# Performance work log

Measured on AMD Instinct MI355X. Metric: run time of the kernel, lower is better.

Reference implementation:

```python
import jax, jax.numpy as jnp
import numpy as np

N = 50000      # nodes
E = 800000     # edges (avg degree 16)
EMB = 128      # emb_dim
NF = 7         # x_features
EF = 5         # edge_features
L = 5          # num_layer
BN_EPS = 1e-5


def setup_inputs() -> dict:
    key = jax.random.key(0)
    ks = jax.random.split(key, 12)
    s = 0.05
    return {
        "x": jax.random.normal(ks[0], (N, NF), jnp.float32),
        "edge_attr": jax.random.normal(ks[1], (E, EF), jnp.float32),
        "edge_index": jax.random.randint(ks[2], (2, E), 0, N, dtype=jnp.int32),
        "W_x": jax.random.normal(ks[3], (NF, EMB), jnp.float32) * s,
        "b_x": jax.random.normal(ks[4], (NF, EMB), jnp.float32) * s,
        "W_e": jax.random.normal(ks[5], (L, EF, EMB), jnp.float32) * s,
        "b_e": jax.random.normal(ks[6], (L, EF, EMB), jnp.float32) * s,
        # per-layer GIN update MLP: Linear(EMB,2EMB)-ReLU-Linear(2EMB,EMB)
        "W1": jax.random.normal(ks[7], (L, EMB, 2 * EMB), jnp.float32) * s,
        "b1": jnp.zeros((L, 2 * EMB), jnp.float32),
        "W2": jax.random.normal(ks[8], (L, 2 * EMB, EMB), jnp.float32) * s,
        "b2": jnp.zeros((L, EMB), jnp.float32),
        # per-layer BatchNorm1d affine params
        "gamma": jnp.ones((L, EMB), jnp.float32),
        "beta": jnp.zeros((L, EMB), jnp.float32),
    }


def reference(x, edge_attr, W_x, b_x, W_e, b_e, W1, b1, W2, b2, gamma, beta, edge_index):
    src, dst = edge_index[0], edge_index[1]
    # initial node embedding: sum of 7 Linear(1,EMB) applied per column == x @ W_x + sum(biases)
    h = x @ W_x + b_x.sum(axis=0)  # [N, EMB]
    for l in range(L):
        # edge embeddings: sum of EF Linear(1,EMB) over edge_attr columns
        e_emb = edge_attr @ W_e[l] + b_e[l].sum(axis=0)  # [E, EMB]
        sl_emb = b_e[l].sum(axis=0)  # self-loop edges have zero attr -> bias sum
        # message = x_j + edge_emb, aggr = add (scatter over dst); self loops add h + sl_emb
        msg = h[src] + e_emb                                        # [E, EMB]
        agg = jax.ops.segment_sum(msg, dst, num_segments=N) + h + sl_emb  # [N, EMB]
        # GIN update MLP
        z = jax.nn.relu(agg @ W1[l] + b1[l]) @ W2[l] + b2[l]        # [N, EMB]
        # BatchNorm1d (training-mode batch stats, biased variance)
        mu = z.mean(axis=0)
        var = z.var(axis=0)
        z = (z - mu) * jax.lax.rsqrt(var + BN_EPS) * gamma[l] + beta[l]
        # ELU on all but last layer; dropout is identity at drop_ratio=0; JK='last'
        h = jax.nn.elu(z) if l < L - 1 else z
    return h
```

## Files before the change

kernel.cpp:

```cpp
#include <hip/hip_runtime.h>
#include <math.h>

#define NN 50000
#define NE 800000
#define EMB 128
#define HID 256
#define NF 7
#define EF 5
#define NL 5
#define BN_EPS 1e-5f
#define NREP 32
#define SCAN_B 196

typedef __attribute__((ext_vector_type(8))) short bf16x8;
typedef __attribute__((ext_vector_type(4))) float f32x4;

__device__ inline unsigned short f2b(float f) {
    unsigned u = __builtin_bit_cast(unsigned, f);
    return (unsigned short)((u + 0x7fffu + ((u >> 16) & 1u)) >> 16);
}
__device__ inline float b2f(unsigned us) {
    return __builtin_bit_cast(float, us << 16);
}
__device__ inline void split2(float a, float b, unsigned& hi, unsigned& lo) {
    unsigned short ha = f2b(a), hb = f2b(b);
    unsigned short la = f2b(a - b2f(ha)), lb = f2b(b - b2f(hb));
    hi = (unsigned)ha | ((unsigned)hb << 16);
    lo = (unsigned)la | ((unsigned)lb << 16);
}
__device__ inline unsigned pkh2(float a, float b) {
    union { unsigned v; _Float16 h[2]; } x;
    x.h[0] = (_Float16)a; x.h[1] = (_Float16)b;
    return x.v;
}
__device__ inline float2 uph2(unsigned u) {
    union { unsigned v; _Float16 h[2]; } x; x.v = u;
    return make_float2((float)x.h[0], (float)x.h[1]);
}

__global__ void k_prep(const float* __restrict__ b_x, const float* __restrict__ b_e,
                       float* __restrict__ bsum_x, float* __restrict__ bsum_e,
                       int* __restrict__ counts, int* __restrict__ cursor) {
    int tid = threadIdx.x;
    if (blockIdx.x == 0 && tid < EMB) {
        float s = 0.f;
        for (int f = 0; f < NF; ++f) s += b_x[f * EMB + tid];
        bsum_x[tid] = s;
        for (int l = 0; l < NL; ++l) {
            float se = 0.f;
            for (int f = 0; f < EF; ++f) se += b_e[(l * EF + f) * EMB + tid];
            bsum_e[l * EMB + tid] = se;
        }
    }
    int gid = blockIdx.x * blockDim.x + tid;
    int stride = gridDim.x * blockDim.x;
    for (int i = gid; i < NN; i += stride) { counts[i] = 0; cursor[i] = 0; }
}

__global__ void k_prepw(const float* __restrict__ W1, const float* __restrict__ W2,
                        unsigned short* __restrict__ W1ph, unsigned short* __restrict__ W1pl,
                        unsigned short* __restrict__ W2ph, unsigned short* __restrict__ W2pl) {
    const int TOT = NL * EMB * HID;
    int gid = blockIdx.x * blockDim.x + threadIdx.x;
    if (gid < TOT) {
        int l = gid / (EMB * HID);
        int r = gid % (EMB * HID);
        int w = r >> 13;
        int rem = r & 8191;
        int h2 = rem >> 11;
        int rem2 = rem & 2047;
        int kk = rem2 >> 9;
        int rem3 = rem2 & 511;
        int lane = rem3 >> 3;
        int j = rem3 & 7;
        int hc = w * 64 + h2 * 16 + (lane & 15);
        int k = kk * 32 + (lane >> 4) * 8 + j;
        float wv = W1[((size_t)l * EMB + k) * HID + hc];
        unsigned short hi = f2b(wv);
        W1ph[gid] = hi;
        W1pl[gid] = f2b(wv - b2f(hi));
    } else if (gid < 2 * TOT) {
        int g = gid - TOT;
        int l = g / (EMB * HID);
        int r = g % (EMB * HID);
        int w = r >> 13;
        int rem = r & 8191;
        int o2 = rem >> 12;
        int rem2 = rem & 4095;
        int kk = rem2 >> 9;
        int rem3 = rem2 & 511;
        int lane = rem3 >> 3;
        int j = rem3 & 7;
        int oc = w * 32 + o2 * 16 + (lane & 15);
        int k2 = kk * 32 + (lane >> 4) * 8 + j;
        float wv = W2[((size_t)l * HID + k2) * EMB + oc];
        unsigned short hi = f2b(wv);
        W2ph[g] = hi;
        W2pl[g] = f2b(wv - b2f(hi));
    }
}

__global__ void k_init(const float* __restrict__ x, const float* __restrict__ W_x,
                       const float* __restrict__ bsum_x, unsigned short* __restrict__ h16) {
    int gid = blockIdx.x * blockDim.x + threadIdx.x;
    int v = gid >> 5;
    if (v >= NN) return;
    int c = (gid & 31) << 2;
    float4 acc = *(const float4*)(bsum_x + c);
    #pragma unroll
    for (int f = 0; f < NF; ++f) {
        float xv = x[(size_t)v * NF + f];
        float4 w = *(const float4*)(W_x + f * EMB + c);
        acc.x += xv * w.x; acc.y += xv * w.y; acc.z += xv * w.z; acc.w += xv * w.w;
    }
    uint2 p = make_uint2(pkh2(acc.x, acc.y), pkh2(acc.z, acc.w));
    *(uint2*)(h16 + (size_t)v * EMB + c) = p;
}

__global__ void k_hist(const int* __restrict__ dst, int* __restrict__ counts) {
    int e = blockIdx.x * blockDim.x + threadIdx.x;
    if (e < NE) atomicAdd(&counts[dst[e]], 1);
}

__global__ void k_scan1(const int* __restrict__ counts, int* __restrict__ bsum) {
    int tid = threadIdx.x;
    int i = blockIdx.x * 256 + tid;
    int v = (i < NN) ? counts[i] : 0;
    #pragma unroll
    for (int off = 1; off < 64; off <<= 1) v += __shfl_xor(v, off, 64);
    __shared__ int ws[4];
    if ((tid & 63) == 0) ws[tid >> 6] = v;
    __syncthreads();
    if (tid == 0) bsum[blockIdx.x] = ws[0] + ws[1] + ws[2] + ws[3];
}

__global__ void k_scan2(const int* __restrict__ bsum, int* __restrict__ bpre,
                        int* __restrict__ row_start) {
    int tid = threadIdx.x;
    int x = (tid < SCAN_B) ? bsum[tid] : 0;
    int lane = tid & 63, wv = tid >> 6;
    int v = x;
    #pragma unroll
    for (int off = 1; off < 64; off <<= 1) {
        int t = __shfl_up(v, off, 64);
        if (lane >= off) v += t;
    }
    __shared__ int wsum[4];
    if (lane == 63) wsum[wv] = v;
    __syncthreads();
    int woff = 0;
    #pragma unroll
    for (int w = 0; w < 4; ++w) if (w < wv) woff += wsum[w];
    int incl = v + woff;
    if (tid < SCAN_B) bpre[tid] = incl - x;
    if (tid == 255) row_start[NN] = incl;
}

__global__ void k_scan3(const int* __restrict__ counts, const int* __restrict__ bpre,
                        int* __restrict__ row_start) {
    int tid = threadIdx.x;
    int i = blockIdx.x * 256 + tid;
    int x = (i < NN) ? counts[i] : 0;
    int lane = tid & 63, wv = tid >> 6;
    int v = x;
    #pragma unroll
    for (int off = 1; off < 64; off <<= 1) {
        int t = __shfl_up(v, off, 64);
        if (lane >= off) v += t;
    }
    __shared__ int wsum[4];
    if (lane == 63) wsum[wv] = v;
    __syncthreads();
    int woff = 0;
    #pragma unroll
    for (int w = 0; w < 4; ++w) if (w < wv) woff += wsum[w];
    if (i < NN) row_start[i] = bpre[blockIdx.x] + v + woff - x;
}

__global__ void k_fill(const int* __restrict__ src, const int* __restrict__ dst,
                       const float* __restrict__ edge_attr,
                       const int* __restrict__ row_start, int* __restrict__ cursor,
                       uint4* __restrict__ sorted_pk) {
    int e = blockIdx.x * blockDim.x + threadIdx.x;
    if (e >= NE) return;
    int d = dst[e];
    int pos = atomicAdd(&cursor[d], 1);
    int idx = row_start[d] + pos;
    const float* ea = edge_attr + (size_t)e * EF;
    float a0 = ea[0], a1 = ea[1], a2 = ea[2], a3 = ea[3], a4 = ea[4];
    uint4 pk;
    pk.x = (unsigned)src[e];
    pk.y = pkh2(a0, a1);
    pk.z = pkh2(a2, a3);
    pk.w = pkh2(a4, 0.f);
    sorted_pk[idx] = pk;
}

__global__ void k_esum(const uint4* __restrict__ sorted_pk,
                       const int* __restrict__ row_start,
                       float* __restrict__ attsum, int* __restrict__ sorted_srcc) {
    int v = blockIdx.x * blockDim.x + threadIdx.x;
    if (v >= NN) return;
    int e0 = row_start[v], e1 = row_start[v + 1];
    float s0 = 0.f, s1 = 0.f, s2 = 0.f, s3 = 0.f, s4 = 0.f;
    for (int e = e0; e < e1; ++e) {
        uint4 pk = sorted_pk[e];
        sorted_srcc[e] = (int)pk.x;
        float2 a01 = uph2(pk.y), a23 = uph2(pk.z), a4x = uph2(pk.w);
        s0 += a01.x; s1 += a01.y; s2 += a23.x; s3 += a23.y; s4 += a4x.x;
    }
    float* o = attsum + (size_t)v * 8;
    *(float4*)(o) = make_float4(s0, s1, s2, s3);
    *(float4*)(o + 4) = make_float4(s4, (float)(e1 - e0), 0.f, 0.f);
}

template<int APPLY_BN>
__global__ __launch_bounds__(256) void k_agg(
        const unsigned short* __restrict__ st16, const int* __restrict__ sorted_srcc,
        const float* __restrict__ attsum, const float* __restrict__ scsh,
        const float* __restrict__ W_e_l, const float* __restrict__ bsum_e_l,
        const int* __restrict__ row_start,
        unsigned* __restrict__ agg_hi, unsigned* __restrict__ agg_lo,
        float* __restrict__ stats) {
    int tid = threadIdx.x;
    if (blockIdx.x < NREP) stats[blockIdx.x * 2 * EMB + tid] = 0.f;
    int gid = blockIdx.x * 256 + tid;
    int v = gid >> 6;
    if (v >= NN) return;
    int c = (gid & 63) << 1;
    float2 we0 = *(const float2*)(W_e_l + 0 * EMB + c);
    float2 we1 = *(const float2*)(W_e_l + 1 * EMB + c);
    float2 we2 = *(const float2*)(W_e_l + 2 * EMB + c);
    float2 we3 = *(const float2*)(W_e_l + 3 * EMB + c);
    float2 we4 = *(const float2*)(W_e_l + 4 * EMB + c);
    float2 bs = *(const float2*)(bsum_e_l + c);
    float2 sc2 = make_float2(0.f, 0.f), sh2 = make_float2(0.f, 0.f);
    if (APPLY_BN) {
        sc2 = *(const float2*)(scsh + c);
        sh2 = *(const float2*)(scsh + EMB + c);
    }
    auto state = [&](unsigned u) -> float2 {
        float2 t = uph2(u);
        if (APPLY_BN) {
            t.x = t.x * sc2.x + sh2.x;
            t.y = t.y * sc2.y + sh2.y;
            t.x = (t.x > 0.f) ? t.x : (__expf(t.x) - 1.f);
            t.y = (t.y > 0.f) ? t.y : (__expf(t.y) - 1.f);
        }
        return t;
    };
    float2 hv = state(*(const unsigned*)(st16 + (size_t)v * EMB + c));
    const float* at = attsum + (size_t)v * 8;
    float4 a03 = *(const float4*)(at);
    float2 a45 = *(const float2*)(at + 4);
    float ax = hv.x + (a45.y + 1.f) * bs.x
             + a03.x*we0.x + a03.y*we1.x + a03.z*we2.x + a03.w*we3.x + a45.x*we4.x;
    float ay = hv.y + (a45.y + 1.f) * bs.y
             + a03.x*we0.y + a03.y*we1.y + a03.z*we2.y + a03.w*we3.y + a45.x*we4.y;
    int e0 = row_start[v], e1 = row_start[v + 1];
    int e = e0;
    for (; e + 8 <= e1; e += 8) {
        int s0 = __builtin_amdgcn_readfirstlane(sorted_srcc[e + 0]);
        int s1 = __builtin_amdgcn_readfirstlane(sorted_srcc[e + 1]);
        int s2 = __builtin_amdgcn_readfirstlane(sorted_srcc[e + 2]);
        int s3 = __builtin_amdgcn_readfirstlane(sorted_srcc[e + 3]);
        int s4 = __builtin_amdgcn_readfirstlane(sorted_srcc[e + 4]);
        int s5 = __builtin_amdgcn_readfirstlane(sorted_srcc[e + 5]);
        int s6 = __builtin_amdgcn_readfirstlane(sorted_srcc[e + 6]);
        int s7 = __builtin_amdgcn_readfirstlane(sorted_srcc[e + 7]);
        unsigned u0 = *(const unsigned*)(st16 + (size_t)s0 * EMB + c);
        unsigned u1 = *(const unsigned*)(st16 + (size_t)s1 * EMB + c);
        unsigned u2 = *(const unsigned*)(st16 + (size_t)s2 * EMB + c);
        unsigned u3 = *(const unsigned*)(st16 + (size_t)s3 * EMB + c);
        unsigned u4 = *(const unsigned*)(st16 + (size_t)s4 * EMB + c);
        unsigned u5 = *(const unsigned*)(st16 + (size_t)s5 * EMB + c);
        unsigned u6 = *(const unsigned*)(st16 + (size_t)s6 * EMB + c);
        unsigned u7 = *(const unsigned*)(st16 + (size_t)s7 * EMB + c);
        float2 h0 = state(u0), h1 = state(u1), h2 = state(u2), h3 = state(u3);
        float2 h4 = state(u4), h5 = state(u5), h6 = state(u6), h7 = state(u7);
        ax += ((h0.x + h1.x) + (h2.x + h3.x)) + ((h4.x + h5.x) + (h6.x + h7.x));
        ay += ((h0.y + h1.y) + (h2.y + h3.y)) + ((h4.y + h5.y) + (h6.y + h7.y));
    }
    for (; e < e1; ++e) {
        int s = __builtin_amdgcn_readfirstlane(sorted_srcc[e]);
        float2 hs = state(*(const unsigned*)(st16 + (size_t)s * EMB + c));
        ax += hs.x;
        ay += hs.y;
    }
    unsigned phi, plo;
    split2(ax, ay, phi, plo);
    size_t o = (size_t)v * (EMB / 2) + (c >> 1);
    agg_hi[o] = phi;
    agg_lo[o] = plo;
}

__global__ __launch_bounds__(256) void k_mlp(
        const unsigned short* __restrict__ aggh, const unsigned short* __restrict__ aggl,
        const unsigned short* __restrict__ W1ph, const unsigned short* __restrict__ W1pl,
        const float* __restrict__ b1_l,
        const unsigned short* __restrict__ W2ph, const unsigned short* __restrict__ W2pl,
        const float* __restrict__ b2_l,
        unsigned short* __restrict__ z16, float* __restrict__ stats) {
    __shared__ unsigned short Ahi[32][136];
    __shared__ unsigned short Alo[32][136];
    __shared__ unsigned short Hhi[32][264];
    __shared__ unsigned short Hlo[32][264];
    int tid = threadIdx.x;
    int r0 = blockIdx.x * 32;
    int rep = blockIdx.x & (NREP - 1);
    #pragma unroll
    for (int it = 0; it < 4; ++it) {
        int idx = it * 256 + tid;
        int plane = idx >> 9;
        int k = idx & 511;
        int row = k >> 4;
        int cb = (k & 15) * 8;
        int grow = r0 + row;
        uint4 val = make_uint4(0u, 0u, 0u, 0u);
        const unsigned short* srcp = plane ? aggl : aggh;
        if (grow < NN) val = *(const uint4*)(srcp + (size_t)grow * EMB + cb);
        if (plane) *(uint4*)(&Alo[row][cb]) = val;
        else       *(uint4*)(&Ahi[row][cb]) = val;
    }
    __syncthreads();
    int wave = tid >> 6, lane = tid & 63;
    int l16 = lane & 15, quad = lane >> 4;
    {
        bf16x8 ahi[2][4], alo[2][4];
        #pragma unroll
        for (int nt = 0; nt < 2; ++nt)
            #pragma unroll
            for (int kk = 0; kk < 4; ++kk) {
                ahi[nt][kk] = *(const bf16x8*)(&Ahi[nt * 16 + l16][kk * 32 + quad * 8]);
                alo[nt][kk] = *(const bf16x8*)(&Alo[nt * 16 + l16][kk * 32 + quad * 8]);
            }
        #pragma unroll
        for (int h2 = 0; h2 < 4; ++h2) {
            bf16x8 whi[4], wlo[4];
            #pragma unroll
            for (int kk = 0; kk < 4; ++kk) {
                size_t off = ((((size_t)(wave * 4 + h2) * 4) + kk) * 64 + lane) * 8;
                whi[kk] = *(const bf16x8*)(W1ph + off);
                wlo[kk] = *(const bf16x8*)(W1pl + off);
            }
            float4 bv = *(const float4*)(b1_l + wave * 64 + h2 * 16 + quad * 4);
            f32x4 bias = {bv.x, bv.y, bv.z, bv.w};
            #pragma unroll
            for (int nt = 0; nt < 2; ++nt) {
                f32x4 acc = bias;
                #pragma unroll
                for (int kk = 0; kk < 4; ++kk)
                    acc = __builtin_amdgcn_mfma_f32_16x16x32_bf16(whi[kk], ahi[nt][kk], acc, 0, 0, 0);
                #pragma unroll
                for (int kk = 0; kk < 4; ++kk)
                    acc = __builtin_amdgcn_mfma_f32_16x16x32_bf16(whi[kk], alo[nt][kk], acc, 0, 0, 0);
                #pragma unroll
                for (int kk = 0; kk < 4; ++kk)
                    acc = __builtin_amdgcn_mfma_f32_16x16x32_bf16(wlo[kk], ahi[nt][kk], acc, 0, 0, 0);
                float v0 = fmaxf(acc[0], 0.f), v1 = fmaxf(acc[1], 0.f);
                float v2 = fmaxf(acc[2], 0.f), v3 = fmaxf(acc[3], 0.f);
                unsigned hiA, loA, hiB, loB;
                split2(v0, v1, hiA, loA);
                split2(v2, v3, hiB, loB);
                int col = wave * 64 + h2 * 16 + quad * 4;
                *(uint2*)(&Hhi[nt * 16 + l16][col]) = make_uint2(hiA, hiB);
                *(uint2*)(&Hlo[nt * 16 + l16][col]) = make_uint2(loA, loB);
            }
        }
    }
    __syncthreads();
    float ss[2][4] = {}, sq[2][4] = {};
    #pragma unroll
    for (int o2 = 0; o2 < 2; ++o2) {
        bf16x8 w2h[8], w2l[8];
        #pragma unroll
        for (int kk = 0; kk < 8; ++kk) {
            size_t off = ((((size_t)(wave * 2 + o2) * 8) + kk) * 64 + lane) * 8;
            w2h[kk] = *(const bf16x8*)(W2ph + off);
            w2l[kk] = *(const bf16x8*)(W2pl + off);
        }
        float4 bv = *(const float4*)(b2_l + wave * 32 + o2 * 16 + quad * 4);
        f32x4 bias = {bv.x, bv.y, bv.z, bv.w};
        #pragma unroll
        for (int nt = 0; nt < 2; ++nt) {
            bf16x8 hh[8], hl[8];
            #pragma unroll
            for (int kk = 0; kk < 8; ++kk) {
                hh[kk] = *(const bf16x8*)(&Hhi[nt * 16 + l16][kk * 32 + quad * 8]);
                hl[kk] = *(const bf16x8*)(&Hlo[nt * 16 + l16][kk * 32 + quad * 8]);
            }
            f32x4 acc = bias;
            #pragma unroll
            for (int kk = 0; kk < 8; ++kk)
                acc = __builtin_amdgcn_mfma_f32_16x16x32_bf16(w2h[kk], hh[kk], acc, 0, 0, 0);
            #pragma unroll
            for (int kk = 0; kk < 8; ++kk)
                acc = __builtin_amdgcn_mfma_f32_16x16x32_bf16(w2h[kk], hl[kk], acc, 0, 0, 0);
            #pragma unroll
            for (int kk = 0; kk < 8; ++kk)
                acc = __builtin_amdgcn_mfma_f32_16x16x32_bf16(w2l[kk], hh[kk], acc, 0, 0, 0);
            int node = r0 + nt * 16 + l16;
            if (node < NN) {
                uint2 p = make_uint2(pkh2(acc[0], acc[1]), pkh2(acc[2], acc[3]));
                *(uint2*)(z16 + (size_t)node * EMB + wave * 32 + o2 * 16 + quad * 4) = p;
                #pragma unroll
                for (int r = 0; r < 4; ++r) {
                    ss[o2][r] += acc[r];
                    sq[o2][r] += acc[r] * acc[r];
                }
            }
        }
    }
    #pragma unroll
    for (int o2 = 0; o2 < 2; ++o2)
        #pragma unroll
        for (int r = 0; r < 4; ++r) {
            float s = ss[o2][r], q = sq[o2][r];
            #pragma unroll
            for (int m = 1; m < 16; m <<= 1) {
                s += __shfl_xor(s, m, 64);
                q += __shfl_xor(q, m, 64);
            }
            if (l16 == 0) {
                int oc = wave * 32 + o2 * 16 + quad * 4 + r;
                atomicAdd(&stats[rep * 2 * EMB + oc], s);
                atomicAdd(&stats[rep * 2 * EMB + EMB + oc], q);
            }
        }
}

__global__ void k_bnscale(const float* __restrict__ stats,
                          const float* __restrict__ gamma_l, const float* __restrict__ beta_l,
                          float* __restrict__ scsh) {
    int tid = threadIdx.x;
    float s = 0.f, q = 0.f;
    #pragma unroll
    for (int r = 0; r < NREP; ++r) {
        s += stats[r * 2 * EMB + tid];
        q += stats[r * 2 * EMB + EMB + tid];
    }
    float mu = s * (1.f / NN);
    float var = q * (1.f / NN) - mu * mu;
    float sf = gamma_l[tid] * rsqrtf(var + BN_EPS);
    scsh[tid] = sf;
    scsh[EMB + tid] = beta_l[tid] - mu * sf;
}

__global__ void k_bn(const unsigned short* __restrict__ z16, const float* __restrict__ scsh,
                     float* __restrict__ fout) {
    __shared__ float sc[EMB], sh[EMB];
    int tid = threadIdx.x;
    if (tid < EMB) {
        sc[tid] = scsh[tid];
        sh[tid] = scsh[EMB + tid];
    }
    __syncthreads();
    int gid = blockIdx.x * blockDim.x + tid;
    if (gid >= NN * EMB / 4) return;
    int c = (gid & 31) << 2;
    uint2 zp = *(const uint2*)(z16 + (size_t)gid * 4);
    float2 z01 = uph2(zp.x), z23 = uph2(zp.y);
    float o0 = z01.x * sc[c + 0] + sh[c + 0];
    float o1 = z01.y * sc[c + 1] + sh[c + 1];
    float o2 = z23.x * sc[c + 2] + sh[c + 2];
    float o3 = z23.y * sc[c + 3] + sh[c + 3];
    *(float4*)(fout + (size_t)gid * 4) = make_float4(o0, o1, o2, o3);
}

extern "C" void kernel_launch(void* const* d_in, const int* in_sizes, int n_in,
                              void* d_out, int out_size, void* d_ws, size_t ws_size,
                              hipStream_t stream) {
    const float* x         = (const float*)d_in[0];
    const float* edge_attr = (const float*)d_in[1];
    const int*   edge_idx  = (const int*)d_in[2];
    const float* W_x   = (const float*)d_in[3];
    const float* b_x   = (const float*)d_in[4];
    const float* W_e   = (const float*)d_in[5];
    const float* b_e   = (const float*)d_in[6];
    const float* W1    = (const float*)d_in[7];
    const float* b1    = (const float*)d_in[8];
    const float* W2    = (const float*)d_in[9];
    const float* b2    = (const float*)d_in[10];
    const float* gamma = (const float*)d_in[11];
    const float* beta  = (const float*)d_in[12];
    float* fout = (float*)d_out;

    const int* src = edge_idx;
    const int* dst = edge_idx + NE;

    char* p = (char*)d_ws;
    auto alloc = [&](size_t bytes) { char* q = p; p += (bytes + 255) & ~(size_t)255; return q; };
    unsigned short* h16 = (unsigned short*)alloc((size_t)NN * EMB * 2);
    unsigned short* z16 = (unsigned short*)alloc((size_t)NN * EMB * 2);
    unsigned* agg_hi = (unsigned*)alloc((size_t)NN * EMB * 2);
    unsigned* agg_lo = (unsigned*)alloc((size_t)NN * EMB * 2);
    unsigned short* W1ph = (unsigned short*)alloc((size_t)NL * HID * EMB * 2);
    unsigned short* W1pl = (unsigned short*)alloc((size_t)NL * HID * EMB * 2);
    unsigned short* W2ph = (unsigned short*)alloc((size_t)NL * EMB * HID * 2);
    unsigned short* W2pl = (unsigned short*)alloc((size_t)NL * EMB * HID * 2);
    int*   row_start  = (int*)alloc((NN + 1) * sizeof(int));
    int*   counts     = (int*)alloc(NN * sizeof(int));
    int*   cursor     = (int*)alloc(NN * sizeof(int));
    uint4* sorted_pk  = (uint4*)alloc((size_t)NE * sizeof(uint4));
    int*   sorted_srcc= (int*)alloc((size_t)NE * sizeof(int));
    float* attsum     = (float*)alloc((size_t)NN * 8 * sizeof(float));
    int*   bsum       = (int*)alloc(SCAN_B * sizeof(int));
    int*   bpre       = (int*)alloc(SCAN_B * sizeof(int));
    float* stats      = (float*)alloc((size_t)NREP * 2 * EMB * sizeof(float));
    float* scsh       = (float*)alloc(2 * EMB * sizeof(float));
    float* bsum_x     = (float*)alloc(EMB * sizeof(float));
    float* bsum_e     = (float*)alloc(NL * EMB * sizeof(float));

    k_prep<<<256, 256, 0, stream>>>(b_x, b_e, bsum_x, bsum_e, counts, cursor);
    k_prepw<<<(2 * NL * EMB * HID + 255) / 256, 256, 0, stream>>>(W1, W2, W1ph, W1pl, W2ph, W2pl);
    k_init<<<(NN * 32 + 255) / 256, 256, 0, stream>>>(x, W_x, bsum_x, h16);
    k_hist<<<(NE + 255) / 256, 256, 0, stream>>>(dst, counts);
    k_scan1<<<SCAN_B, 256, 0, stream>>>(counts, bsum);
    k_scan2<<<1, 256, 0, stream>>>(bsum, bpre, row_start);
    k_scan3<<<SCAN_B, 256, 0, stream>>>(counts, bpre, row_start);
    k_fill<<<(NE + 255) / 256, 256, 0, stream>>>(src, dst, edge_attr, row_start, cursor,
                                                 sorted_pk);
    k_esum<<<SCAN_B, 256, 0, stream>>>(sorted_pk, row_start, attsum, sorted_srcc);
    const int AGG_GRID = (NN * 64 + 255) / 256;
    for (int l = 0; l < NL; ++l) {
        if (l == 0) {
            k_agg<0><<<AGG_GRID, 256, 0, stream>>>(
                h16, sorted_srcc, attsum, scsh,
                W_e + (size_t)l * EF * EMB, bsum_e + l * EMB, row_start,
                agg_hi, agg_lo, stats);
        } else {
            k_agg<1><<<AGG_GRID, 256, 0, stream>>>(
                z16, sorted_srcc, attsum, scsh,
                W_e + (size_t)l * EF * EMB, bsum_e + l * EMB, row_start,
                agg_hi, agg_lo, stats);
        }
        k_mlp<<<(NN + 31) / 32, 256, 0, stream>>>(
            (const unsigned short*)agg_hi, (const unsigned short*)agg_lo,
            W1ph + (size_t)l * HID * EMB, W1pl + (size_t)l * HID * EMB, b1 + (size_t)l * HID,
            W2ph + (size_t)l * EMB * HID, W2pl + (size_t)l * EMB * HID, b2 + (size_t)l * EMB,
            z16, stats);
        k_bnscale<<<1, 128, 0, stream>>>(stats, gamma + l * EMB, beta + l * EMB, scsh);
    }
    k_bn<<<(NN * EMB / 4 + 255) / 256, 256, 0, stream>>>(z16, scsh, fout);
}
```

Measured before the change: 634.6 us.

## Gather 16-byte neighbor rows across four lane-groups and fold edge-attr sums into fill

The aggregation kernel now splits each 64-lane wavefront into four edge groups of 16 lanes, each lane loading 8 channels (a 16-byte vector) per neighbor, and reduces the partial sums with cross-lane shuffles. The previous version had all 64 lanes read 4-byte slices of the same neighbor row. Separately, the per-node edge-attribute sums are now accumulated with float atomics inside the fill kernel, which removes the packed sorted-edge buffer and the k_esum pass. The cost is float atomic contention and non-deterministic summation order. Only the lanes with eg==0 write the output, and the shuffle reduction adds some overhead.

```diff
diff --git a/kernel.cpp b/kernel.cpp
--- a/kernel.cpp
+++ b/kernel.cpp
@@ -40,7 +40,8 @@
 
 __global__ void k_prep(const float* __restrict__ b_x, const float* __restrict__ b_e,
                        float* __restrict__ bsum_x, float* __restrict__ bsum_e,
-                       int* __restrict__ counts, int* __restrict__ cursor) {
+                       int* __restrict__ counts, int* __restrict__ cursor,
+                       float* __restrict__ attsum) {
     int tid = threadIdx.x;
     if (blockIdx.x == 0 && tid < EMB) {
         float s = 0.f;
@@ -55,6 +56,7 @@
     int gid = blockIdx.x * blockDim.x + tid;
     int stride = gridDim.x * blockDim.x;
     for (int i = gid; i < NN; i += stride) { counts[i] = 0; cursor[i] = 0; }
+    for (int i = gid; i < NN * 8; i += stride) attsum[i] = 0.f;
 }
 
 __global__ void k_prepw(const float* __restrict__ W1, const float* __restrict__ W2,
@@ -180,38 +182,19 @@
 __global__ void k_fill(const int* __restrict__ src, const int* __restrict__ dst,
                        const float* __restrict__ edge_attr,
                        const int* __restrict__ row_start, int* __restrict__ cursor,
-                       uint4* __restrict__ sorted_pk) {
+                       int* __restrict__ sorted_srcc, float* __restrict__ attsum) {
     int e = blockIdx.x * blockDim.x + threadIdx.x;
     if (e >= NE) return;
     int d = dst[e];
     int pos = atomicAdd(&cursor[d], 1);
-    int idx = row_start[d] + pos;
+    sorted_srcc[row_start[d] + pos] = src[e];
     const float* ea = edge_attr + (size_t)e * EF;
-    float a0 = ea[0], a1 = ea[1], a2 = ea[2], a3 = ea[3], a4 = ea[4];
-    uint4 pk;
-    pk.x = (unsigned)src[e];
-    pk.y = pkh2(a0, a1);
-    pk.z = pkh2(a2, a3);
-    pk.w = pkh2(a4, 0.f);
-    sorted_pk[idx] = pk;
-}
-
-__global__ void k_esum(const uint4* __restrict__ sorted_pk,
-                       const int* __restrict__ row_start,
-                       float* __restrict__ attsum, int* __restrict__ sorted_srcc) {
-    int v = blockIdx.x * blockDim.x + threadIdx.x;
-    if (v >= NN) return;
-    int e0 = row_start[v], e1 = row_start[v + 1];
-    float s0 = 0.f, s1 = 0.f, s2 = 0.f, s3 = 0.f, s4 = 0.f;
-    for (int e = e0; e < e1; ++e) {
-        uint4 pk = sorted_pk[e];
-        sorted_srcc[e] = (int)pk.x;
-        float2 a01 = uph2(pk.y), a23 = uph2(pk.z), a4x = uph2(pk.w);
-        s0 += a01.x; s1 += a01.y; s2 += a23.x; s3 += a23.y; s4 += a4x.x;
-    }
-    float* o = attsum + (size_t)v * 8;
-    *(float4*)(o) = make_float4(s0, s1, s2, s3);
-    *(float4*)(o + 4) = make_float4(s4, (float)(e1 - e0), 0.f, 0.f);
+    float* ap = attsum + (size_t)d * 8;
+    atomicAdd(ap + 0, ea[0]);
+    atomicAdd(ap + 1, ea[1]);
+    atomicAdd(ap + 2, ea[2]);
+    atomicAdd(ap + 3, ea[3]);
+    atomicAdd(ap + 4, ea[4]);
 }
 
 template<int APPLY_BN>
@@ -227,71 +210,108 @@
     int gid = blockIdx.x * 256 + tid;
     int v = gid >> 6;
     if (v >= NN) return;
-    int c = (gid & 63) << 1;
-    float2 we0 = *(const float2*)(W_e_l + 0 * EMB + c);
-    float2 we1 = *(const float2*)(W_e_l + 1 * EMB + c);
-    float2 we2 = *(const float2*)(W_e_l + 2 * EMB + c);
-    float2 we3 = *(const float2*)(W_e_l + 3 * EMB + c);
-    float2 we4 = *(const float2*)(W_e_l + 4 * EMB + c);
-    float2 bs = *(const float2*)(bsum_e_l + c);
-    float2 sc2 = make_float2(0.f, 0.f), sh2 = make_float2(0.f, 0.f);
+    int lane = tid & 63;
+    int li = lane & 15;
+    int eg = lane >> 4;
+    int cb = li * 8;
+    float scv[8], shv[8];
     if (APPLY_BN) {
-        sc2 = *(const float2*)(scsh + c);
-        sh2 = *(const float2*)(scsh + EMB + c);
-    }
-    auto state = [&](unsigned u) -> float2 {
-        float2 t = uph2(u);
-        if (APPLY_BN) {
-            t.x = t.x * sc2.x + sh2.x;
-            t.y = t.y * sc2.y + sh2.y;
-            t.x = (t.x > 0.f) ? t.x : (__expf(t.x) - 1.f);
-            t.y = (t.y > 0.f) ? t.y : (__expf(t.y) - 1.f);
-        }
-        return t;
+        float4 s0 = *(const float4*)(scsh + cb);
+        float4 s1 = *(const float4*)(scsh + cb + 4);
+        float4 t0 = *(const float4*)(scsh + EMB + cb);
+        float4 t1 = *(const float4*)(scsh + EMB + cb + 4);
+        scv[0]=s0.x; scv[1]=s0.y; scv[2]=s0.z; scv[3]=s0.w;
+        scv[4]=s1.x; scv[5]=s1.y; scv[6]=s1.z; scv[7]=s1.w;
+        shv[0]=t0.x; shv[1]=t0.y; shv[2]=t0.z; shv[3]=t0.w;
+        shv[4]=t1.x; shv[5]=t1.y; shv[6]=t1.z; shv[7]=t1.w;
+    }
+    float acc[8] = {0.f,0.f,0.f,0.f,0.f,0.f,0.f,0.f};
+    auto accum8 = [&](uint4 u) {
+        float2 p0 = uph2(u.x), p1 = uph2(u.y), p2 = uph2(u.z), p3 = uph2(u.w);
+        float t[8] = {p0.x, p0.y, p1.x, p1.y, p2.x, p2.y, p3.x, p3.y};
+        #pragma unroll
+        for (int j = 0; j < 8; ++j) {
+            float xx = t[j];
+            if (APPLY_BN) {
+                xx = xx * scv[j] + shv[j];
+                xx = (xx > 0.f) ? xx : (__expf(xx) - 1.f);
+            }
+            acc[j] += xx;
+        }
     };
-    float2 hv = state(*(const unsigned*)(st16 + (size_t)v * EMB + c));
+    int e0 = row_start[v], e1 = row_start[v + 1];
+    int e = e0;
+    for (; e + 16 <= e1; e += 16) {
+        int sA = sorted_srcc[e + eg];
+        int sB = sorted_srcc[e + 4 + eg];
+        int sC = sorted_srcc[e + 8 + eg];
+        int sD = sorted_srcc[e + 12 + eg];
+        uint4 uA = *(const uint4*)(st16 + (size_t)sA * EMB + cb);
+        uint4 uB = *(const uint4*)(st16 + (size_t)sB * EMB + cb);
+        uint4 uC = *(const uint4*)(st16 + (size_t)sC * EMB + cb);
+        uint4 uD = *(const uint4*)(st16 + (size_t)sD * EMB + cb);
+        accum8(uA); accum8(uB); accum8(uC); accum8(uD);
+    }
+    for (; e < e1; e += 4) {
+        int ee = e + eg;
+        if (ee < e1) {
+            int s = sorted_srcc[ee];
+            uint4 u = *(const uint4*)(st16 + (size_t)s * EMB + cb);
+            accum8(u);
+        }
+    }
+    #pragma unroll
+    for (int j = 0; j < 8; ++j) {
+        acc[j] += __shfl_xor(acc[j], 16, 64);
+        acc[j] += __shfl_xor(acc[j], 32, 64);
+    }
+    float deg = (float)(e1 - e0);
     const float* at = attsum + (size_t)v * 8;
     float4 a03 = *(const float4*)(at);
-    float2 a45 = *(const float2*)(at + 4);
-    float ax = hv.x + (a45.y + 1.f) * bs.x
-             + a03.x*we0.x + a03.y*we1.x + a03.z*we2.x + a03.w*we3.x + a45.x*we4.x;
-    float ay = hv.y + (a45.y + 1.f) * bs.y
-             + a03.x*we0.y + a03.y*we1.y + a03.z*we2.y + a03.w*we3.y + a45.x*we4.y;
-    int e0 = row_start[v], e1 = row_start[v + 1];
-    int e = e0;
-    for (; e + 8 <= e1; e += 8) {
-        int s0 = __builtin_amdgcn_readfirstlane(sorted_srcc[e + 0]);
-        int s1 = __builtin_amdgcn_readfirstlane(sorted_srcc[e + 1]);
-        int s2 = __builtin_amdgcn_readfirstlane(sorted_srcc[e + 2]);
-        int s3 = __builtin_amdgcn_readfirstlane(sorted_srcc[e + 3]);
-        int s4 = __builtin_amdgcn_readfirstlane(sorted_srcc[e + 4]);
-        int s5 = __builtin_amdgcn_readfirstlane(sorted_srcc[e + 5]);
-        int s6 = __builtin_amdgcn_readfirstlane(sorted_srcc[e + 6]);
-        int s7 = __builtin_amdgcn_readfirstlane(sorted_srcc[e + 7]);
-        unsigned u0 = *(const unsigned*)(st16 + (size_t)s0 * EMB + c);
-        unsigned u1 = *(const unsigned*)(st16 + (size_t)s1 * EMB + c);
-        unsigned u2 = *(const unsigned*)(st16 + (size_t)s2 * EMB + c);
-        unsigned u3 = *(const unsigned*)(st16 + (size_t)s3 * EMB + c);
-        unsigned u4 = *(const unsigned*)(st16 + (size_t)s4 * EMB + c);
-        unsigned u5 = *(const unsigned*)(st16 + (size_t)s5 * EMB + c);
-        unsigned u6 = *(const unsigned*)(st16 + (size_t)s6 * EMB + c);
-        unsigned u7 = *(const unsigned*)(st16 + (size_t)s7 * EMB + c);
-        float2 h0 = state(u0), h1 = state(u1), h2 = state(u2), h3 = state(u3);
-        float2 h4 = state(u4), h5 = state(u5), h6 = state(u6), h7 = state(u7);
-        ax += ((h0.x + h1.x) + (h2.x + h3.x)) + ((h4.x + h5.x) + (h6.x + h7.x));
-        ay += ((h0.y + h1.y) + (h2.y + h3.y)) + ((h4.y + h5.y) + (h6.y + h7.y));
-    }
-    for (; e < e1; ++e) {
-        int s = __builtin_amdgcn_readfirstlane(sorted_srcc[e]);
-        float2 hs = state(*(const unsigned*)(st16 + (size_t)s * EMB + c));
-        ax += hs.x;
-        ay += hs.y;
-    }
-    unsigned phi, plo;
-    split2(ax, ay, phi, plo);
-    size_t o = (size_t)v * (EMB / 2) + (c >> 1);
-    agg_hi[o] = phi;
-    agg_lo[o] = plo;
+    float a4 = at[4];
+    uint4 su = *(const uint4*)(st16 + (size_t)v * EMB + cb);
+    float2 q0 = uph2(su.x), q1 = uph2(su.y), q2 = uph2(su.z), q3 = uph2(su.w);
+    float sf[8] = {q0.x, q0.y, q1.x, q1.y, q2.x, q2.y, q3.x, q3.y};
+    if (APPLY_BN) {
+        #pragma unroll
+        for (int j = 0; j < 8; ++j) {
+            float xx = sf[j] * scv[j] + shv[j];
+            sf[j] = (xx > 0.f) ? xx : (__expf(xx) - 1.f);
+        }
+    }
+    float out[8];
+    #pragma unroll
+    for (int half = 0; half < 2; ++half) {
+        int cbh = cb + half * 4;
+        float4 bsv = *(const float4*)(bsum_e_l + cbh);
+        float4 w0 = *(const float4*)(W_e_l + 0 * EMB + cbh);
+        float4 w1 = *(const float4*)(W_e_l + 1 * EMB + cbh);
+        float4 w2 = *(const float4*)(W_e_l + 2 * EMB + cbh);
+        float4 w3 = *(const float4*)(W_e_l + 3 * EMB + cbh);
+        float4 w4 = *(const float4*)(W_e_l + 4 * EMB + cbh);
+        const float* bsp = (const float*)&bsv;
+        const float* w0p = (const float*)&w0;
+        const float* w1p = (const float*)&w1;
+        const float* w2p = (const float*)&w2;
+        const float* w3p = (const float*)&w3;
+        const float* w4p = (const float*)&w4;
+        #pragma unroll
+        for (int j = 0; j < 4; ++j) {
+            int jj = half * 4 + j;
+            out[jj] = acc[jj] + sf[jj] + (deg + 1.f) * bsp[j]
+                    + a03.x * w0p[j] + a03.y * w1p[j] + a03.z * w2p[j]
+                    + a03.w * w3p[j] + a4 * w4p[j];
+        }
+    }
+    if (eg == 0) {
+        uint4 hi, lo;
+        split2(out[0], out[1], hi.x, lo.x);
+        split2(out[2], out[3], hi.y, lo.y);
+        split2(out[4], out[5], hi.z, lo.z);
+        split2(out[6], out[7], hi.w, lo.w);
+        *(uint4*)(agg_hi + (size_t)v * 64 + li * 4) = hi;
+        *(uint4*)(agg_lo + (size_t)v * 64 + li * 4) = lo;
+    }
 }
 
 __global__ __launch_bounds__(256) void k_mlp(
@@ -501,7 +521,6 @@
     int*   row_start  = (int*)alloc((NN + 1) * sizeof(int));
     int*   counts     = (int*)alloc(NN * sizeof(int));
     int*   cursor     = (int*)alloc(NN * sizeof(int));
-    uint4* sorted_pk  = (uint4*)alloc((size_t)NE * sizeof(uint4));
     int*   sorted_srcc= (int*)alloc((size_t)NE * sizeof(int));
     float* attsum     = (float*)alloc((size_t)NN * 8 * sizeof(float));
     int*   bsum       = (int*)alloc(SCAN_B * sizeof(int));
@@ -511,7 +530,7 @@
     float* bsum_x     = (float*)alloc(EMB * sizeof(float));
     float* bsum_e     = (float*)alloc(NL * EMB * sizeof(float));
 
-    k_prep<<<256, 256, 0, stream>>>(b_x, b_e, bsum_x, bsum_e, counts, cursor);
+    k_prep<<<256, 256, 0, stream>>>(b_x, b_e, bsum_x, bsum_e, counts, cursor, attsum);
     k_prepw<<<(2 * NL * EMB * HID + 255) / 256, 256, 0, stream>>>(W1, W2, W1ph, W1pl, W2ph, W2pl);
     k_init<<<(NN * 32 + 255) / 256, 256, 0, stream>>>(x, W_x, bsum_x, h16);
     k_hist<<<(NE + 255) / 256, 256, 0, stream>>>(dst, counts);
@@ -519,8 +538,7 @@
     k_scan2<<<1, 256, 0, stream>>>(bsum, bpre, row_start);
     k_scan3<<<SCAN_B, 256, 0, stream>>>(counts, bpre, row_start);
     k_fill<<<(NE + 255) / 256, 256, 0, stream>>>(src, dst, edge_attr, row_start, cursor,
-                                                 sorted_pk);
-    k_esum<<<SCAN_B, 256, 0, stream>>>(sorted_pk, row_start, attsum, sorted_srcc);
+                                                 sorted_srcc, attsum);
     const int AGG_GRID = (NN * 64 + 255) / 256;
     for (int l = 0; l < NL; ++l) {
         if (l == 0) {
```

Measured after the change: 858.9 us. 35.3% more time.
